# Optimization experiments

Measured on AMD Instinct MI355X. Metric: run time of the kernel, lower is better.

## Reference

```python
import jax, jax.numpy as jnp
import numpy as np

T, B, D, H = 256, 64, 1024, 1024


def _linear_params(key, fan_in, shape_w, shape_b):
    kw, kb = jax.random.split(key)
    bound = 1.0 / np.sqrt(fan_in)
    W = jax.random.uniform(kw, shape_w, jnp.float32, -bound, bound)
    b = jax.random.uniform(kb, shape_b, jnp.float32, -bound, bound)
    return W, b


def setup_inputs() -> dict:
    key = jax.random.key(0)
    ks = jax.random.split(key, 6)
    x = jax.random.normal(ks[0], (T, B, D), jnp.float32)
    hidden = jnp.zeros((B, H), jnp.float32)
    cell = jnp.zeros((B, H), jnp.float32)
    W_in, b_in = _linear_params(ks[1], D, (H, D), (H,))
    W_hid, b_hid = _linear_params(ks[2], H, (H, H), (H,))
    # 4 gates (i, f, g, o), each with an x-path and h-path hidden->hidden Linear
    Wx_g, bx_g = _linear_params(ks[3], H, (4, H, H), (4, H))
    Wh_g, bh_g = _linear_params(ks[4], H, (4, H, H), (4, H))
    return {"x": x, "hidden": hidden, "cell": cell,
            "W_in": W_in, "b_in": b_in, "W_hid": W_hid, "b_hid": b_hid,
            "Wx_g": Wx_g, "bx_g": bx_g, "Wh_g": Wh_g, "bh_g": bh_g}


def reference(x, hidden, cell, W_in, b_in, W_hid, b_hid, Wx_g, bx_g, Wh_g, bh_g):
    # input_layer / hidden_layer projections, then 4 gate Linears per path,
    # mirroring the many-small-Linear LSTM cell of the torch module.
    def step(carry, x_t):
        h, c = carry
        x2h = x_t @ W_in.T + b_in          # [B, H]
        h2h = h @ W_hid.T + b_hid          # [B, H]
        g = (jnp.einsum('ghk,bk->gbh', Wx_g, x2h) + bx_g[:, None, :]
             + jnp.einsum('ghk,bk->gbh', Wh_g, h2h) + bh_g[:, None, :])  # [4, B, H]
        i = jax.nn.sigmoid(g[0])
        f = jax.nn.sigmoid(g[1])
        gg = jnp.tanh(g[2])
        o = jax.nn.sigmoid(g[3])
        c_new = f * c + i * gg
        h_new = o * jnp.tanh(c_new)
        return (h_new, c_new), None

    (h, c), _ = jax.lax.scan(step, (hidden, cell), x)
    return (h, c)
```

## Files before the change

kernel.cpp:

```cpp
#include <hip/hip_runtime.h>

typedef __attribute__((ext_vector_type(8))) short short8;
typedef __attribute__((ext_vector_type(4))) float f32x4;

#define SEQ_BLOCKS 64

__device__ __forceinline__ unsigned short f2bf(float f) {
  unsigned u = __float_as_uint(f);
  u = u + 0x7fffu + ((u >> 16) & 1u);
  return (unsigned short)(u >> 16);
}
__device__ __forceinline__ unsigned short f2h(float f) {
  _Float16 h = (_Float16)f;
  unsigned short r;
  __builtin_memcpy(&r, &h, 2);
  return r;
}
__device__ __forceinline__ float h2f(unsigned short u) {
  _Float16 h;
  __builtin_memcpy(&h, &u, 2);
  return (float)h;
}
__device__ __forceinline__ void gload16(const void* g, void* l) {
  __builtin_amdgcn_global_load_lds(
      (const __attribute__((address_space(1))) unsigned int*)g,
      (__attribute__((address_space(3))) unsigned int*)l, 16, 0, 0);
}
__device__ __forceinline__ float fast_sigmoid(float x) {
  return 1.0f / (1.0f + __expf(-x));
}
__device__ __forceinline__ float fast_tanh(float x) {
  return 2.0f / (1.0f + __expf(-2.0f * x)) - 1.0f;
}
__device__ __forceinline__ short8 load_h16(const unsigned short* p) {
  union { unsigned long long u[2]; short8 s; } r;
  r.u[0] = __hip_atomic_load((const unsigned long long*)p, __ATOMIC_RELAXED,
                             __HIP_MEMORY_SCOPE_AGENT);
  r.u[1] = __hip_atomic_load(((const unsigned long long*)p) + 1, __ATOMIC_RELAXED,
                             __HIP_MEMORY_SCOPE_AGENT);
  return r.s;
}

__global__ void k_conv_bf16(const float* __restrict__ in, unsigned short* __restrict__ out) {
  size_t i = ((size_t)blockIdx.x * 256 + threadIdx.x) * 4;
  float4 v = *(const float4*)(in + i);
  unsigned short o[4] = {f2bf(v.x), f2bf(v.y), f2bf(v.z), f2bf(v.w)};
  *(uint2*)(out + i) = *(const uint2*)o;
}

__global__ void k_h0t(const float* __restrict__ hidden, unsigned short* __restrict__ hT) {
  int sb = blockIdx.x;
  int row = threadIdx.x >> 2, c4 = (threadIdx.x & 3) * 4;
  float4 v = *(const float4*)(hidden + (size_t)row * 1024 + sb * 16 + c4);
  unsigned short o[4] = {f2bf(v.x), f2bf(v.y), f2bf(v.z), f2bf(v.w)};
  unsigned long long u;
  __builtin_memcpy(&u, o, 8);
  *(unsigned long long*)(hT + (size_t)sb * 1024 + row * 16 + c4) = u;
}

__global__ void k_transpose(const float* __restrict__ in, unsigned short* __restrict__ out,
                            int R, int C) {
  __shared__ float tile[32][33];
  int bx = blockIdx.x * 32, by = blockIdx.y * 32;
  int tx = threadIdx.x & 31, ty = threadIdx.x >> 5;
  for (int i = 0; i < 32; i += 8)
    tile[ty + i][tx] = in[(size_t)(by + ty + i) * C + bx + tx];
  __syncthreads();
  for (int i = 0; i < 32; i += 8)
    out[(size_t)(bx + ty + i) * R + by + tx] = f2bf(tile[tx][ty + i]);
}

template<int OUTMODE>
__global__ __launch_bounds__(256) void k_gemm_bt(
    const unsigned short* __restrict__ A, const unsigned short* __restrict__ B,
    unsigned short* __restrict__ C, const float* __restrict__ bias,
    int M, int N, int K) {
  __shared__ unsigned short As[128 * 32];
  __shared__ unsigned short Bs[128 * 32];
  const int tid = threadIdx.x;
  const int wv = tid >> 6, l = tid & 63;
  const int m0 = blockIdx.y * 128, n0 = blockIdx.x * 128;
  const int wr = (wv >> 1) * 64, wc = (wv & 1) * 64;
  f32x4 acc[4][4] = {};
  for (int k0 = 0; k0 < K; k0 += 32) {
#pragma unroll
    for (int j = 0; j < 2; ++j) {
      int c = wv * 128 + j * 64 + l;
      int row = c >> 2, kc = (c & 3) * 8;
      gload16(A + (size_t)(m0 + row) * K + k0 + kc, (char*)As + c * 16);
      gload16(B + (size_t)(n0 + row) * K + k0 + kc, (char*)Bs + c * 16);
    }
    __syncthreads();
    short8 af[4], bfr[4];
#pragma unroll
    for (int rf = 0; rf < 4; ++rf)
      af[rf] = *(const short8*)(As + (wr + rf * 16 + (l & 15)) * 32 + (l >> 4) * 8);
#pragma unroll
    for (int cf = 0; cf < 4; ++cf)
      bfr[cf] = *(const short8*)(Bs + (wc + cf * 16 + (l & 15)) * 32 + (l >> 4) * 8);
#pragma unroll
    for (int rf = 0; rf < 4; ++rf)
#pragma unroll
      for (int cf = 0; cf < 4; ++cf)
        acc[rf][cf] = __builtin_amdgcn_mfma_f32_16x16x32_bf16(af[rf], bfr[cf], acc[rf][cf], 0, 0, 0);
    __syncthreads();
  }
#pragma unroll
  for (int cf = 0; cf < 4; ++cf) {
    int col = n0 + wc + cf * 16 + (l & 15);
    float bv = bias ? bias[col] : 0.0f;
#pragma unroll
    for (int rf = 0; rf < 4; ++rf) {
#pragma unroll
      for (int i = 0; i < 4; ++i) {
        int row = m0 + wr + rf * 16 + (l >> 4) * 4 + i;
        float v = acc[rf][cf][i] + bv;
        if (OUTMODE == 0) {
          C[(size_t)row * N + col] = f2bf(v);
        } else {
          int t = row >> 6, b = row & 63;
          int g = col >> 10, c = col & 1023;
          size_t idx = (size_t)(t * 64 + (c >> 4)) * 4096 + (g * 64 + b) * 16 + (c & 15);
          C[idx] = f2h(v);
        }
      }
    }
  }
}

__global__ void k_bias(const float* __restrict__ Wxg, const float* __restrict__ bxg,
                       const float* __restrict__ b_in, const float* __restrict__ Whg,
                       const float* __restrict__ bhg, const float* __restrict__ b_hid,
                       float* __restrict__ gbias) {
  int col = blockIdx.x * 64 + (threadIdx.x >> 2);
  int p = threadIdx.x & 3;
  const float* wx = Wxg + (size_t)col * 1024;
  const float* wh = Whg + (size_t)col * 1024;
  float s = 0.f;
  for (int k = p * 256; k < p * 256 + 256; ++k)
    s += wx[k] * b_in[k] + wh[k] * b_hid[k];
  s += __shfl_down(s, 2, 4);
  s += __shfl_down(s, 1, 4);
  if (p == 0) gbias[col] = s + bxg[col] + bhg[col];
}

__global__ __launch_bounds__(256, 1) void k_lstm_seq(
    const unsigned short* __restrict__ GX2,
    const unsigned short* __restrict__ Whc,
    const float* __restrict__ cell,
    unsigned short* __restrict__ hT,
    float* __restrict__ out,
    unsigned* __restrict__ flags) {
  __shared__ float pbuf[34816];
  const int tid = threadIdx.x;
  const int wv = tid >> 6, l = tid & 63;
  const int bid = blockIdx.x;
  const int a = l & 15, q = l >> 4;

  short8 w[4][8];
#pragma unroll
  for (int ct = 0; ct < 4; ++ct)
#pragma unroll
    for (int u = 0; u < 8; ++u)
      w[ct][u] = *(const short8*)(
          Whc + (size_t)(ct * 1024 + bid * 16 + a) * 1024 + wv * 256 + u * 32 + q * 8);

  const int eb = tid >> 2;
  const int ej = (tid & 3) * 4;
  float c_reg[4];
  {
    float4 c4 = *(const float4*)(cell + (size_t)eb * 1024 + bid * 16 + ej);
    c_reg[0] = c4.x; c_reg[1] = c4.y; c_reg[2] = c4.z; c_reg[3] = c4.w;
  }

  const size_t abase = (size_t)(wv * 16 + (q >> 1)) * 1024 + a * 16 + (q & 1) * 8;
  const unsigned* pollp = flags + wv * 32 + a;

  for (int t = 0; t < 256; ++t) {
    const unsigned short* chunk = GX2 + ((size_t)t * 64 + bid) * 4096;
    unsigned long long gxu[4];
#pragma unroll
    for (int g = 0; g < 4; ++g)
      gxu[g] = *(const unsigned long long*)(chunk + (g * 64 + eb) * 16 + ej);

    if (t > 0) {
      const unsigned tgt = (unsigned)t;
      for (;;) {
        unsigned v = __hip_atomic_load(pollp, __ATOMIC_RELAXED, __HIP_MEMORY_SCOPE_AGENT);
        if (__all((int)(v >= tgt))) break;
        __builtin_amdgcn_s_sleep(1);
      }
      __builtin_amdgcn_fence(__ATOMIC_ACQUIRE, "workgroup");
    }

    const unsigned short* hb = hT + ((size_t)(t & 3) << 16) + abase;
    short8 afr[4][8];
#pragma unroll
    for (int u = 0; u < 8; ++u)
#pragma unroll
      for (int rt = 0; rt < 4; ++rt)
        afr[rt][u] = load_h16(hb + u * 2048 + rt * 256);

    f32x4 acc[4][4] = {};
#pragma unroll
    for (int u = 0; u < 8; ++u)
#pragma unroll
      for (int rt = 0; rt < 4; ++rt)
#pragma unroll
        for (int ct = 0; ct < 4; ++ct)
          acc[rt][ct] = __builtin_amdgcn_mfma_f32_16x16x32_bf16(afr[rt][u], w[ct][u],
                                                                acc[rt][ct], 0, 0, 0);

    const int pb = (t & 1) * 17408 + wv * 4352;
#pragma unroll
    for (int rt = 0; rt < 4; ++rt)
#pragma unroll
      for (int ct = 0; ct < 4; ++ct) {
        int gc = a * 4 + ct;
        int b0 = (rt * 16 + q * 4) ^ ((((gc) >> 3) & 3) << 2);
        *(f32x4*)&pbuf[pb + gc * 68 + b0] = acc[rt][ct];
      }
    __syncthreads();

    const int pr = (t & 1) * 17408;
    float sg[4][4];
#pragma unroll
    for (int g = 0; g < 4; ++g) {
      unsigned short gx4[4];
      __builtin_memcpy(gx4, &gxu[g], 8);
#pragma unroll
      for (int i = 0; i < 4; ++i) {
        int gc = (ej + i) * 4 + g;
        int bx = eb ^ ((((gc) >> 3) & 3) << 2);
        float s = pbuf[pr + 0 * 4352 + gc * 68 + bx] + pbuf[pr + 1 * 4352 + gc * 68 + bx] +
                  pbuf[pr + 2 * 4352 + gc * 68 + bx] + pbuf[pr + 3 * 4352 + gc * 68 + bx];
        sg[g][i] = s + h2f(gx4[i]);
      }
    }
    float hnew[4];
#pragma unroll
    for (int i = 0; i < 4; ++i) {
      float ig = fast_sigmoid(sg[0][i]);
      float fg = fast_sigmoid(sg[1][i]);
      float gg = fast_tanh(sg[2][i]);
      float og = fast_sigmoid(sg[3][i]);
      c_reg[i] = fg * c_reg[i] + ig * gg;
      hnew[i] = og * fast_tanh(c_reg[i]);
    }

    if (t == 255) {
      float4 h4 = {hnew[0], hnew[1], hnew[2], hnew[3]};
      float4 c4 = {c_reg[0], c_reg[1], c_reg[2], c_reg[3]};
      *(float4*)(out + (size_t)eb * 1024 + bid * 16 + ej) = h4;
      *(float4*)(out + 65536 + (size_t)eb * 1024 + bid * 16 + ej) = c4;
    } else {
      unsigned short hs[4] = {f2bf(hnew[0]), f2bf(hnew[1]), f2bf(hnew[2]), f2bf(hnew[3])};
      unsigned long long hv;
      __builtin_memcpy(&hv, hs, 8);
      __hip_atomic_store(
          (unsigned long long*)(hT + ((size_t)((t + 1) & 3) << 16) + (size_t)bid * 1024 +
                                eb * 16 + ej),
          hv, __ATOMIC_RELAXED, __HIP_MEMORY_SCOPE_AGENT);
      asm volatile("s_waitcnt vmcnt(0)" ::: "memory");
      __syncthreads();
      if (tid == 0)
        __hip_atomic_store(&flags[(bid >> 4) * 32 + (bid & 15)], (unsigned)(t + 1),
                           __ATOMIC_RELAXED, __HIP_MEMORY_SCOPE_AGENT);
    }
  }
}

extern "C" void kernel_launch(void* const* d_in, const int* in_sizes, int n_in,
                              void* d_out, int out_size, void* d_ws, size_t ws_size,
                              hipStream_t stream) {
  const float* x      = (const float*)d_in[0];
  const float* hidden = (const float*)d_in[1];
  const float* cell   = (const float*)d_in[2];
  const float* W_in   = (const float*)d_in[3];
  const float* b_in   = (const float*)d_in[4];
  const float* W_hid  = (const float*)d_in[5];
  const float* b_hid  = (const float*)d_in[6];
  const float* Wx_g   = (const float*)d_in[7];
  const float* bx_g   = (const float*)d_in[8];
  const float* Wh_g   = (const float*)d_in[9];
  const float* bh_g   = (const float*)d_in[10];
  float* out = (float*)d_out;

  char* ws = (char*)d_ws;
  unsigned short* GX2   = (unsigned short*)(ws);
  unsigned short* Xbf   = (unsigned short*)(ws + 134217728);
  unsigned short* WxGb  = (unsigned short*)(ws + 167772160);
  unsigned short* WhGb  = (unsigned short*)(ws + 176160768);
  unsigned short* WinT  = (unsigned short*)(ws + 184549376);
  unsigned short* WhidT = (unsigned short*)(ws + 186646528);
  unsigned short* Wxc   = (unsigned short*)(ws + 188743680);
  unsigned short* Whc   = (unsigned short*)(ws + 197132288);
  float*          gbias = (float*)(ws + 205520896);
  unsigned short* hT    = (unsigned short*)(ws + 134217728);
  unsigned*       flags = (unsigned*)(ws + 184549376);

  k_conv_bf16<<<16384, 256, 0, stream>>>(x, Xbf);
  k_conv_bf16<<<4096, 256, 0, stream>>>(Wx_g, WxGb);
  k_conv_bf16<<<4096, 256, 0, stream>>>(Wh_g, WhGb);
  k_transpose<<<dim3(32, 32), 256, 0, stream>>>(W_in, WinT, 1024, 1024);
  k_transpose<<<dim3(32, 32), 256, 0, stream>>>(W_hid, WhidT, 1024, 1024);
  k_gemm_bt<0><<<dim3(8, 32), 256, 0, stream>>>(WxGb, WinT, Wxc, nullptr, 4096, 1024, 1024);
  k_gemm_bt<0><<<dim3(8, 32), 256, 0, stream>>>(WhGb, WhidT, Whc, nullptr, 4096, 1024, 1024);
  k_bias<<<64, 256, 0, stream>>>(Wx_g, bx_g, b_in, Wh_g, bh_g, b_hid, gbias);
  k_gemm_bt<1><<<dim3(32, 128), 256, 0, stream>>>(Xbf, Wxc, GX2, gbias, 16384, 4096, 1024);
  k_h0t<<<64, 256, 0, stream>>>(hidden, hT);
  hipMemsetAsync(flags, 0, 512, stream);
  k_lstm_seq<<<SEQ_BLOCKS, 256, 0, stream>>>(GX2, Whc, cell, hT, out, flags);
}
```

Measured before the change: 2.206 ms.

## Replace flag-based step barrier with poisoned per-step hidden-state buffers

Instead of a 4-deep ring of hidden-state buffers guarded by per-block progress flags, each timestep now gets its own buffer, pre-filled with an all-ones poison pattern. Consumers load their h fragments and re-poll only the 64-bit words that still hold poison, so data arrival itself acts as the signal. This removes the waitcnt, block barrier and flag store on the producer side, and the separate flag poll on the consumer side. The cost is a 32 MB memset before the recurrence and a reliance on bf16 data never equalling the poison pattern (all-ones is a NaN encoding, so normal values should not match).

```diff
diff --git a/kernel.cpp b/kernel.cpp
--- a/kernel.cpp
+++ b/kernel.cpp
@@ -32,13 +32,11 @@
 __device__ __forceinline__ float fast_tanh(float x) {
   return 2.0f / (1.0f + __expf(-2.0f * x)) - 1.0f;
 }
-__device__ __forceinline__ short8 load_h16(const unsigned short* p) {
-  union { unsigned long long u[2]; short8 s; } r;
-  r.u[0] = __hip_atomic_load((const unsigned long long*)p, __ATOMIC_RELAXED,
-                             __HIP_MEMORY_SCOPE_AGENT);
-  r.u[1] = __hip_atomic_load(((const unsigned long long*)p) + 1, __ATOMIC_RELAXED,
-                             __HIP_MEMORY_SCOPE_AGENT);
-  return r.s;
+__device__ __forceinline__ unsigned long long ld_u64(const unsigned long long* p) {
+  return __hip_atomic_load(p, __ATOMIC_RELAXED, __HIP_MEMORY_SCOPE_AGENT);
+}
+__device__ __forceinline__ void st_u64(unsigned long long* p, unsigned long long v) {
+  __hip_atomic_store(p, v, __ATOMIC_RELAXED, __HIP_MEMORY_SCOPE_AGENT);
 }
 
 __global__ void k_conv_bf16(const float* __restrict__ in, unsigned short* __restrict__ out) {
@@ -148,14 +146,14 @@
     const unsigned short* __restrict__ GX2,
     const unsigned short* __restrict__ Whc,
     const float* __restrict__ cell,
-    unsigned short* __restrict__ hT,
-    float* __restrict__ out,
-    unsigned* __restrict__ flags) {
+    unsigned short* __restrict__ hstep,
+    float* __restrict__ out) {
   __shared__ float pbuf[34816];
   const int tid = threadIdx.x;
   const int wv = tid >> 6, l = tid & 63;
   const int bid = blockIdx.x;
   const int a = l & 15, q = l >> 4;
+  const unsigned long long POISON = ~0ULL;
 
   short8 w[4][8];
 #pragma unroll
@@ -174,7 +172,6 @@
   }
 
   const size_t abase = (size_t)(wv * 16 + (q >> 1)) * 1024 + a * 16 + (q & 1) * 8;
-  const unsigned* pollp = flags + wv * 32 + a;
 
   for (int t = 0; t < 256; ++t) {
     const unsigned short* chunk = GX2 + ((size_t)t * 64 + bid) * 4096;
@@ -183,33 +180,48 @@
     for (int g = 0; g < 4; ++g)
       gxu[g] = *(const unsigned long long*)(chunk + (g * 64 + eb) * 16 + ej);
 
-    if (t > 0) {
-      const unsigned tgt = (unsigned)t;
-      for (;;) {
-        unsigned v = __hip_atomic_load(pollp, __ATOMIC_RELAXED, __HIP_MEMORY_SCOPE_AGENT);
-        if (__all((int)(v >= tgt))) break;
-        __builtin_amdgcn_s_sleep(1);
-      }
-      __builtin_amdgcn_fence(__ATOMIC_ACQUIRE, "workgroup");
-    }
-
-    const unsigned short* hb = hT + ((size_t)(t & 3) << 16) + abase;
-    short8 afr[4][8];
+    const unsigned short* hb = hstep + ((size_t)t << 16) + abase;
+    unsigned long long ck[8][4][2];
 #pragma unroll
     for (int u = 0; u < 8; ++u)
 #pragma unroll
-      for (int rt = 0; rt < 4; ++rt)
-        afr[rt][u] = load_h16(hb + u * 2048 + rt * 256);
+      for (int rt = 0; rt < 4; ++rt) {
+        const unsigned long long* p = (const unsigned long long*)(hb + u * 2048 + rt * 256);
+        ck[u][rt][0] = ld_u64(p);
+        ck[u][rt][1] = ld_u64(p + 1);
+      }
+    for (;;) {
+      unsigned nbad = 0;
+#pragma unroll
+      for (int u = 0; u < 8; ++u)
+#pragma unroll
+        for (int rt = 0; rt < 4; ++rt)
+          nbad += (ck[u][rt][0] == POISON) + (ck[u][rt][1] == POISON);
+      if (!__any((int)nbad)) break;
+      __builtin_amdgcn_s_sleep(1);
+#pragma unroll
+      for (int u = 0; u < 8; ++u)
+#pragma unroll
+        for (int rt = 0; rt < 4; ++rt) {
+          const unsigned long long* p = (const unsigned long long*)(hb + u * 2048 + rt * 256);
+          if (ck[u][rt][0] == POISON) ck[u][rt][0] = ld_u64(p);
+          if (ck[u][rt][1] == POISON) ck[u][rt][1] = ld_u64(p + 1);
+        }
+    }
 
     f32x4 acc[4][4] = {};
 #pragma unroll
     for (int u = 0; u < 8; ++u)
 #pragma unroll
-      for (int rt = 0; rt < 4; ++rt)
+      for (int rt = 0; rt < 4; ++rt) {
+        union { unsigned long long d[2]; short8 s; } fb;
+        fb.d[0] = ck[u][rt][0];
+        fb.d[1] = ck[u][rt][1];
 #pragma unroll
         for (int ct = 0; ct < 4; ++ct)
-          acc[rt][ct] = __builtin_amdgcn_mfma_f32_16x16x32_bf16(afr[rt][u], w[ct][u],
+          acc[rt][ct] = __builtin_amdgcn_mfma_f32_16x16x32_bf16(fb.s, w[ct][u],
                                                                 acc[rt][ct], 0, 0, 0);
+      }
 
     const int pb = (t & 1) * 17408 + wv * 4352;
 #pragma unroll
@@ -257,15 +269,9 @@
       unsigned short hs[4] = {f2bf(hnew[0]), f2bf(hnew[1]), f2bf(hnew[2]), f2bf(hnew[3])};
       unsigned long long hv;
       __builtin_memcpy(&hv, hs, 8);
-      __hip_atomic_store(
-          (unsigned long long*)(hT + ((size_t)((t + 1) & 3) << 16) + (size_t)bid * 1024 +
-                                eb * 16 + ej),
-          hv, __ATOMIC_RELAXED, __HIP_MEMORY_SCOPE_AGENT);
-      asm volatile("s_waitcnt vmcnt(0)" ::: "memory");
-      __syncthreads();
-      if (tid == 0)
-        __hip_atomic_store(&flags[(bid >> 4) * 32 + (bid & 15)], (unsigned)(t + 1),
-                           __ATOMIC_RELAXED, __HIP_MEMORY_SCOPE_AGENT);
+      st_u64((unsigned long long*)(hstep + ((size_t)(t + 1) << 16) + (size_t)bid * 1024 +
+                                   eb * 16 + ej),
+             hv);
     }
   }
 }
@@ -296,8 +302,7 @@
   unsigned short* Wxc   = (unsigned short*)(ws + 188743680);
   unsigned short* Whc   = (unsigned short*)(ws + 197132288);
   float*          gbias = (float*)(ws + 205520896);
-  unsigned short* hT    = (unsigned short*)(ws + 134217728);
-  unsigned*       flags = (unsigned*)(ws + 184549376);
+  unsigned short* hstep = (unsigned short*)(ws + 134217728);
 
   k_conv_bf16<<<16384, 256, 0, stream>>>(x, Xbf);
   k_conv_bf16<<<4096, 256, 0, stream>>>(Wx_g, WxGb);
@@ -308,7 +313,7 @@
   k_gemm_bt<0><<<dim3(8, 32), 256, 0, stream>>>(WhGb, WhidT, Whc, nullptr, 4096, 1024, 1024);
   k_bias<<<64, 256, 0, stream>>>(Wx_g, bx_g, b_in, Wh_g, bh_g, b_hid, gbias);
   k_gemm_bt<1><<<dim3(32, 128), 256, 0, stream>>>(Xbf, Wxc, GX2, gbias, 16384, 4096, 1024);
-  k_h0t<<<64, 256, 0, stream>>>(hidden, hT);
-  hipMemsetAsync(flags, 0, 512, stream);
-  k_lstm_seq<<<SEQ_BLOCKS, 256, 0, stream>>>(GX2, Whc, cell, hT, out, flags);
-}
+  hipMemsetAsync(hstep, 0xFF, 33685504, stream);
+  k_h0t<<<64, 256, 0, stream>>>(hidden, hstep);
+  k_lstm_seq<<<SEQ_BLOCKS, 256, 0, stream>>>(GX2, Whc, cell, hstep, out);
+}
```

After: 2.379 ms. +7.8%, slower.

## Fuse input-projection GEMM into recurrent kernel with producer/consumer overlap

Applied to the files above, without the earlier changes.

Removes the separate large x-projection GEMM launch and runs it inside the sequential LSTM kernel. Extra workgroups beyond the 64 recurrent blocks pull GEMM tiles from an atomic work counter and write the gate-input layout through an LDS transpose. They then bump per-timestep-pair counters, which the recurrent blocks poll before consuming each step. The aim is to hide the GEMM behind the latency-bound recurrence, at the cost of contention for CUs and memory bandwidth, extra polling, and a reliance on all 256 blocks being co-resident.

```diff
diff --git a/kernel.cpp b/kernel.cpp
--- a/kernel.cpp
+++ b/kernel.cpp
@@ -4,6 +4,7 @@
 typedef __attribute__((ext_vector_type(4))) float f32x4;
 
 #define SEQ_BLOCKS 64
+#define GX_TILES 4096u
 
 __device__ __forceinline__ unsigned short f2bf(float f) {
   unsigned u = __float_as_uint(f);
@@ -32,12 +33,13 @@
 __device__ __forceinline__ float fast_tanh(float x) {
   return 2.0f / (1.0f + __expf(-2.0f * x)) - 1.0f;
 }
+__device__ __forceinline__ unsigned long long ld_u64(const unsigned long long* p) {
+  return __hip_atomic_load(p, __ATOMIC_RELAXED, __HIP_MEMORY_SCOPE_AGENT);
+}
 __device__ __forceinline__ short8 load_h16(const unsigned short* p) {
   union { unsigned long long u[2]; short8 s; } r;
-  r.u[0] = __hip_atomic_load((const unsigned long long*)p, __ATOMIC_RELAXED,
-                             __HIP_MEMORY_SCOPE_AGENT);
-  r.u[1] = __hip_atomic_load(((const unsigned long long*)p) + 1, __ATOMIC_RELAXED,
-                             __HIP_MEMORY_SCOPE_AGENT);
+  r.u[0] = ld_u64((const unsigned long long*)p);
+  r.u[1] = ld_u64(((const unsigned long long*)p) + 1);
   return r.s;
 }
 
@@ -70,11 +72,9 @@
     out[(size_t)(bx + ty + i) * R + by + tx] = f2bf(tile[tx][ty + i]);
 }
 
-template<int OUTMODE>
 __global__ __launch_bounds__(256) void k_gemm_bt(
     const unsigned short* __restrict__ A, const unsigned short* __restrict__ B,
-    unsigned short* __restrict__ C, const float* __restrict__ bias,
-    int M, int N, int K) {
+    unsigned short* __restrict__ C, int M, int N, int K) {
   __shared__ unsigned short As[128 * 32];
   __shared__ unsigned short Bs[128 * 32];
   const int tid = threadIdx.x;
@@ -108,21 +108,12 @@
 #pragma unroll
   for (int cf = 0; cf < 4; ++cf) {
     int col = n0 + wc + cf * 16 + (l & 15);
-    float bv = bias ? bias[col] : 0.0f;
 #pragma unroll
     for (int rf = 0; rf < 4; ++rf) {
 #pragma unroll
       for (int i = 0; i < 4; ++i) {
         int row = m0 + wr + rf * 16 + (l >> 4) * 4 + i;
-        float v = acc[rf][cf][i] + bv;
-        if (OUTMODE == 0) {
-          C[(size_t)row * N + col] = f2bf(v);
-        } else {
-          int t = row >> 6, b = row & 63;
-          int g = col >> 10, c = col & 1023;
-          size_t idx = (size_t)(t * 64 + (c >> 4)) * 4096 + (g * 64 + b) * 16 + (c & 15);
-          C[idx] = f2h(v);
-        }
+        C[(size_t)row * N + col] = f2bf(acc[rf][cf][i]);
       }
     }
   }
@@ -144,17 +135,96 @@
   if (p == 0) gbias[col] = s + bxg[col] + bhg[col];
 }
 
-__global__ __launch_bounds__(256, 1) void k_lstm_seq(
-    const unsigned short* __restrict__ GX2,
+__global__ __launch_bounds__(256, 1) void k_fused(
+    const unsigned short* __restrict__ Xbf,
+    const unsigned short* __restrict__ Wxc,
+    const float* __restrict__ gbias,
+    unsigned short* __restrict__ GX2,
     const unsigned short* __restrict__ Whc,
     const float* __restrict__ cell,
     unsigned short* __restrict__ hT,
     float* __restrict__ out,
-    unsigned* __restrict__ flags) {
-  __shared__ float pbuf[34816];
+    unsigned* __restrict__ flags,
+    unsigned* __restrict__ gxcnt,
+    unsigned* __restrict__ workctr) {
+  __shared__ __align__(16) char smem[139264];
   const int tid = threadIdx.x;
+  const int bid = blockIdx.x;
+
+  if (bid >= SEQ_BLOCKS) {
+    unsigned short* As = (unsigned short*)smem;
+    unsigned short* Bs = As + 128 * 32;
+    unsigned short* T  = (unsigned short*)(smem + 16384);
+    unsigned* tbox = (unsigned*)(smem + 139256);
+    const int wv = tid >> 6, l = tid & 63;
+    const int wr = (wv >> 1) * 64, wc = (wv & 1) * 64;
+    for (;;) {
+      __syncthreads();
+      if (tid == 0)
+        *tbox = __hip_atomic_fetch_add(workctr, 1u, __ATOMIC_RELAXED, __HIP_MEMORY_SCOPE_AGENT);
+      __syncthreads();
+      unsigned tile = *tbox;
+      if (tile >= GX_TILES) break;
+      const int p = tile >> 5, xt = tile & 31;
+      const int m0 = p * 128, n0 = xt * 128;
+      f32x4 acc[4][4] = {};
+      for (int k0 = 0; k0 < 1024; k0 += 32) {
+#pragma unroll
+        for (int j = 0; j < 2; ++j) {
+          int c = wv * 128 + j * 64 + l;
+          int row = c >> 2, kc = (c & 3) * 8;
+          gload16(Xbf + (size_t)(m0 + row) * 1024 + k0 + kc, (char*)As + c * 16);
+          gload16(Wxc + (size_t)(n0 + row) * 1024 + k0 + kc, (char*)Bs + c * 16);
+        }
+        __syncthreads();
+        short8 af[4], bfr[4];
+#pragma unroll
+        for (int rf = 0; rf < 4; ++rf)
+          af[rf] = *(const short8*)(As + (wr + rf * 16 + (l & 15)) * 32 + (l >> 4) * 8);
+#pragma unroll
+        for (int cf = 0; cf < 4; ++cf)
+          bfr[cf] = *(const short8*)(Bs + (wc + cf * 16 + (l & 15)) * 32 + (l >> 4) * 8);
+#pragma unroll
+        for (int rf = 0; rf < 4; ++rf)
+#pragma unroll
+          for (int cf = 0; cf < 4; ++cf)
+            acc[rf][cf] = __builtin_amdgcn_mfma_f32_16x16x32_bf16(af[rf], bfr[cf], acc[rf][cf], 0, 0, 0);
+        __syncthreads();
+      }
+#pragma unroll
+      for (int cf = 0; cf < 4; ++cf) {
+        int cl = wc + cf * 16 + (l & 15);
+        float bv = gbias[n0 + cl];
+#pragma unroll
+        for (int rf = 0; rf < 4; ++rf)
+#pragma unroll
+          for (int i = 0; i < 4; ++i)
+            T[(wr + rf * 16 + (l >> 4) * 4 + i) * 136 + cl] = f2h(acc[rf][cf][i] + bv);
+      }
+      __syncthreads();
+      const int g = xt >> 3, blks0 = (xt & 7) * 8;
+#pragma unroll
+      for (int pp = 0; pp < 8; ++pp) {
+        int s = pp * 2 + (tid >> 7);
+        int t2 = s >> 3, blkL = s & 7;
+        int k = tid & 127, b = k >> 1, half = k & 1;
+        const unsigned long long* src =
+            (const unsigned long long*)(T + (t2 * 64 + b) * 136 + blkL * 16 + half * 8);
+        unsigned long long* dst = (unsigned long long*)(
+            GX2 + ((size_t)((2 * p + t2) * 64 + blks0 + blkL)) * 4096 + g * 1024 + b * 16 + half * 8);
+        __hip_atomic_store(dst, src[0], __ATOMIC_RELAXED, __HIP_MEMORY_SCOPE_AGENT);
+        __hip_atomic_store(dst + 1, src[1], __ATOMIC_RELAXED, __HIP_MEMORY_SCOPE_AGENT);
+      }
+      asm volatile("s_waitcnt vmcnt(0)" ::: "memory");
+      __syncthreads();
+      if (tid == 0)
+        __hip_atomic_fetch_add(&gxcnt[p], 1u, __ATOMIC_RELAXED, __HIP_MEMORY_SCOPE_AGENT);
+    }
+    return;
+  }
+
+  float* pbuf = (float*)smem;
   const int wv = tid >> 6, l = tid & 63;
-  const int bid = blockIdx.x;
   const int a = l & 15, q = l >> 4;
 
   short8 w[4][8];
@@ -175,8 +245,17 @@
 
   const size_t abase = (size_t)(wv * 16 + (q >> 1)) * 1024 + a * 16 + (q & 1) * 8;
   const unsigned* pollp = flags + wv * 32 + a;
+  int gxsafe = 0;
 
   for (int t = 0; t < 256; ++t) {
+    const int pw = t >> 1;
+    while (gxsafe <= pw) {
+      unsigned v = __hip_atomic_load(&gxcnt[gxsafe], __ATOMIC_RELAXED, __HIP_MEMORY_SCOPE_AGENT);
+      if (v >= 32u) ++gxsafe;
+      else __builtin_amdgcn_s_sleep(2);
+    }
+    __builtin_amdgcn_fence(__ATOMIC_ACQUIRE, "workgroup");
+
     const unsigned short* chunk = GX2 + ((size_t)t * 64 + bid) * 4096;
     unsigned long long gxu[4];
 #pragma unroll
@@ -191,6 +270,7 @@
         __builtin_amdgcn_s_sleep(1);
       }
       __builtin_amdgcn_fence(__ATOMIC_ACQUIRE, "workgroup");
+      __builtin_amdgcn_sched_barrier(0);
     }
 
     const unsigned short* hb = hT + ((size_t)(t & 3) << 16) + abase;
@@ -296,19 +376,22 @@
   unsigned short* Wxc   = (unsigned short*)(ws + 188743680);
   unsigned short* Whc   = (unsigned short*)(ws + 197132288);
   float*          gbias = (float*)(ws + 205520896);
-  unsigned short* hT    = (unsigned short*)(ws + 134217728);
-  unsigned*       flags = (unsigned*)(ws + 184549376);
+  unsigned short* hT    = (unsigned short*)(ws + 167772160);
+  unsigned*       ctrl  = (unsigned*)(ws + 184549376);
+  unsigned*       flags = ctrl;
+  unsigned*       gxcnt = ctrl + 256;
+  unsigned*       wctr  = ctrl + 512;
 
   k_conv_bf16<<<16384, 256, 0, stream>>>(x, Xbf);
   k_conv_bf16<<<4096, 256, 0, stream>>>(Wx_g, WxGb);
   k_conv_bf16<<<4096, 256, 0, stream>>>(Wh_g, WhGb);
   k_transpose<<<dim3(32, 32), 256, 0, stream>>>(W_in, WinT, 1024, 1024);
   k_transpose<<<dim3(32, 32), 256, 0, stream>>>(W_hid, WhidT, 1024, 1024);
-  k_gemm_bt<0><<<dim3(8, 32), 256, 0, stream>>>(WxGb, WinT, Wxc, nullptr, 4096, 1024, 1024);
-  k_gemm_bt<0><<<dim3(8, 32), 256, 0, stream>>>(WhGb, WhidT, Whc, nullptr, 4096, 1024, 1024);
+  k_gemm_bt<<<dim3(8, 32), 256, 0, stream>>>(WxGb, WinT, Wxc, 4096, 1024, 1024);
+  k_gemm_bt<<<dim3(8, 32), 256, 0, stream>>>(WhGb, WhidT, Whc, 4096, 1024, 1024);
   k_bias<<<64, 256, 0, stream>>>(Wx_g, bx_g, b_in, Wh_g, bh_g, b_hid, gbias);
-  k_gemm_bt<1><<<dim3(32, 128), 256, 0, stream>>>(Xbf, Wxc, GX2, gbias, 16384, 4096, 1024);
   k_h0t<<<64, 256, 0, stream>>>(hidden, hT);
-  hipMemsetAsync(flags, 0, 512, stream);
-  k_lstm_seq<<<SEQ_BLOCKS, 256, 0, stream>>>(GX2, Whc, cell, hT, out, flags);
-}
+  hipMemsetAsync(ctrl, 0, 4096, stream);
+  k_fused<<<256, 256, 0, stream>>>(Xbf, Wxc, gbias, GX2, Whc, cell, hT, out,
+                                   flags, gxcnt, wctr);
+}
```

Result: faster. 2.017 ms (-8.6%).
